# Performance work log

Measured on AMD Instinct MI355X. Metric: run time of the kernel, lower is better.

## Reference

```python
import jax, jax.numpy as jnp
import numpy as np

B = 64
D_MODEL = 2048
D_SSM = 4096      # expand * d_model
HEADDIM = 64
NHEADS = 64       # D_SSM // HEADDIM
D_STATE = 128
D_IN_PROJ = 2 * D_SSM + 2 * D_STATE + NHEADS  # 8512, d_mlp == 0
ACT_LEVELS = 2 ** (8 - 1) - 1  # 127
W_LEVELS = 2 ** (8 - 1) - 1


def fake_quant(x, levels):
    # symmetric absmax fake-quant along last dim with straight-through estimator
    scale = jnp.max(jnp.abs(x), axis=-1, keepdims=True) / levels
    scale = jnp.where(scale == 0, 1.0, scale)
    q = jnp.round(x / scale) * scale
    return x + jax.lax.stop_gradient(q - x)


def quant_linear(x, W):
    # QuantLinear: fake-quant activations (per row) and weights (per output channel)
    xq = fake_quant(x, ACT_LEVELS)
    Wq = fake_quant(W, W_LEVELS)
    return xq @ Wq.T


def softplus_taylor3(x):
    return jnp.log(2.0) + 0.5 * x + x ** 2 / 8.0 + x ** 3 / 48.0


def exp_taylor5(x):
    return 1.0 + x + x ** 2 / 2.0 + x ** 3 / 6.0 + x ** 4 / 24.0 + x ** 5 / 120.0


def setup_inputs() -> dict:
    key = jax.random.key(0)
    k = jax.random.split(key, 7)
    hidden_states = jax.random.normal(k[0], (B, 1, D_MODEL), dtype=jnp.float32)
    ssm_state = jax.random.normal(k[1], (B, NHEADS, HEADDIM, D_STATE), dtype=jnp.float32) * 0.1
    W_in = jax.random.normal(k[2], (D_IN_PROJ, D_MODEL), dtype=jnp.float32) * (1.0 / np.sqrt(D_MODEL))
    # dt_bias = inverse-softplus of dt ~ LogUniform(1e-3, 1e-1)
    dt = jnp.exp(jax.random.uniform(k[3], (NHEADS,)) * (np.log(0.1) - np.log(0.001)) + np.log(0.001))
    dt_bias = dt + jnp.log(-jnp.expm1(-dt))
    A_log = jnp.log(jax.random.uniform(k[4], (NHEADS,), minval=1.0, maxval=16.0))
    Dp = jnp.ones((D_SSM,), dtype=jnp.float32)
    W_out = jax.random.normal(k[5], (D_MODEL, D_SSM), dtype=jnp.float32) * (1.0 / np.sqrt(D_SSM))
    return {"hidden_states": hidden_states, "ssm_state": ssm_state, "W_in": W_in,
            "dt_bias": dt_bias, "A_log": A_log, "D": Dp, "W_out": W_out}


def reference(hidden_states, ssm_state, W_in, dt_bias, A_log, D, W_out):
    dtype = hidden_states.dtype
    b = hidden_states.shape[0]
    zxbcdt = quant_linear(hidden_states[:, 0, :], W_in)  # [b, 8512]
    z = zxbcdt[:, :D_SSM]
    xBC = zxbcdt[:, D_SSM:2 * D_SSM + 2 * D_STATE]
    dt = zxbcdt[:, -NHEADS:]
    # activation fake-quant on xBC (STE)
    xBC = fake_quant(xBC, ACT_LEVELS)
    x = xBC[:, :D_SSM]                                   # [b, d_ssm]
    Bm = xBC[:, D_SSM:D_SSM + D_STATE]                   # [b, n]
    C = xBC[:, D_SSM + D_STATE:]                         # [b, n]
    A = -jnp.exp(A_log.astype(jnp.float32))              # [h]
    # no_sftplus: piecewise 3rd-order Taylor softplus
    dt = dt + dt_bias.astype(dt.dtype)
    dt = jnp.where(dt < -2.0, 0.0, jnp.where(dt > 2.0, dt, softplus_taylor3(dt)))
    # taylor_exp: clipped 5th-order Taylor exp of dt*A
    dA = jnp.maximum(dt * A, -10000.0)
    scale = jnp.clip(exp_taylor5(dA), 0.0, 1.0)          # [b, h]
    xh = x.reshape(b, NHEADS, HEADDIM)                   # [b, h, p]
    dBx = jnp.einsum('bh,bn,bhp->bhpn', dt, Bm, xh)
    ssm_state = ssm_state * scale[:, :, None, None] + dBx  # [b, h, p, n]
    y = jnp.einsum('bhpn,bn->bhp', ssm_state.astype(dtype), C).reshape(b, D_SSM)
    y = fake_quant(y, ACT_LEVELS)
    y = y + D.astype(dtype) * x                          # per-channel skip (D has d_ssm entries)
    y = y * jax.nn.relu(z)
    y = fake_quant(y, ACT_LEVELS)
    out = quant_linear(y, W_out)                         # [b, d_model]
    return out[:, None, :]
```

## Files before the change

### kernel.cpp

```cpp
#include <hip/hip_runtime.h>


#define B_       64
#define DMODEL   2048
#define DSSM     4096
#define NH       64
#define HD       64
#define DSTATE   128
#define DPROJ    8512
#define XBCLEN   4352
#define KS1      8
#define KS2      16

typedef __attribute__((ext_vector_type(8))) short short8;
typedef __attribute__((ext_vector_type(4))) float floatx4;

__device__ __forceinline__ float blockMax256(float v, float* sm) {
  #pragma unroll
  for (int off = 32; off > 0; off >>= 1)
    v = fmaxf(v, __shfl_xor(v, off, 64));
  __syncthreads();
  if ((threadIdx.x & 63) == 0) sm[threadIdx.x >> 6] = v;
  __syncthreads();
  return fmaxf(fmaxf(sm[0], sm[1]), fmaxf(sm[2], sm[3]));
}

__device__ __forceinline__ float absmax4(float4 v) {
  return fmaxf(fmaxf(fabsf(v.x), fabsf(v.y)), fmaxf(fabsf(v.z), fabsf(v.w)));
}

__device__ __forceinline__ unsigned short bf16_of_int(float q) {
  return (unsigned short)(__float_as_uint(q) >> 16);
}

template<int COLS>
__device__ __forceinline__ void qrow(const float* __restrict__ in,
                                     unsigned short* __restrict__ outq,
                                     float* __restrict__ scales, int r, float* sm) {
  constexpr int NV = COLS / 1024;
  const float4* row = (const float4*)(in + (size_t)r * COLS);
  float4 v[NV];
  float m = 0.f;
  #pragma unroll
  for (int i = 0; i < NV; i++) {
    v[i] = row[threadIdx.x + i * 256];
    m = fmaxf(m, absmax4(v[i]));
  }
  float mx = blockMax256(m, sm);
  float s = mx * (1.0f / 127.0f);
  float rs = (s == 0.f) ? 0.f : 127.0f / mx;
  if (s == 0.f) s = 1.f;
  if (threadIdx.x == 0) scales[r] = s;
  unsigned short* orow = outq + (size_t)r * COLS;
  #pragma unroll
  for (int i = 0; i < NV; i++) {
    int idx = (threadIdx.x + i * 256) * 4;
    ushort4 o;
    o.x = bf16_of_int(rintf(v[i].x * rs));
    o.y = bf16_of_int(rintf(v[i].y * rs));
    o.z = bf16_of_int(rintf(v[i].z * rs));
    o.w = bf16_of_int(rintf(v[i].w * rs));
    *(ushort4*)(orow + idx) = o;
  }
}

__global__ __launch_bounds__(256) void kquant_all(
    const float* __restrict__ hidden, const float* __restrict__ W_in,
    const float* __restrict__ W_out,
    unsigned short* __restrict__ xq, unsigned short* __restrict__ winq,
    unsigned short* __restrict__ woq,
    float* __restrict__ sx, float* __restrict__ swin, float* __restrict__ swo) {
  __shared__ float sm[4];
  int bid = blockIdx.x;
  if (bid < DPROJ)                 qrow<DMODEL>(W_in, winq, swin, bid, sm);
  else if (bid < DPROJ + DMODEL)   qrow<DSSM>(W_out, woq, swo, bid - DPROJ, sm);
  else                             qrow<DMODEL>(hidden, xq, sx, bid - DPROJ - DMODEL, sm);
}

__global__ __launch_bounds__(256) void gemm_q(
    const unsigned short* __restrict__ A, int lda, const float* __restrict__ sA,
    const unsigned short* __restrict__ Bq, int ldb, const float* __restrict__ sB,
    float* __restrict__ Pout, int N, int kchunk) {
  int wave = threadIdx.x >> 6;
  int lane = threadIdx.x & 63;
  int l16 = lane & 15, quad = lane >> 4;
  int n0 = blockIdx.x * 64 + wave * 16;
  int k0 = blockIdx.y * kchunk;
  floatx4 zero = {0.f, 0.f, 0.f, 0.f};
  floatx4 acc[4] = {zero, zero, zero, zero};
  const unsigned short* brow = Bq + (size_t)(n0 + l16) * ldb + quad * 8;
  const unsigned short* arow = A + (size_t)l16 * lda + quad * 8;
  short8 bnext = *(const short8*)(brow + k0);
  short8 anext[4];
  #pragma unroll
  for (int mt = 0; mt < 4; mt++)
    anext[mt] = *(const short8*)(arow + (size_t)mt * 16 * lda + k0);
  for (int k = k0; k < k0 + kchunk; k += 32) {
    short8 bcur = bnext;
    short8 acur[4] = {anext[0], anext[1], anext[2], anext[3]};
    if (k + 32 < k0 + kchunk) {
      bnext = *(const short8*)(brow + k + 32);
      #pragma unroll
      for (int mt = 0; mt < 4; mt++)
        anext[mt] = *(const short8*)(arow + (size_t)mt * 16 * lda + k + 32);
    }
    #pragma unroll
    for (int mt = 0; mt < 4; mt++)
      acc[mt] = __builtin_amdgcn_mfma_f32_16x16x32_bf16(acur[mt], bcur, acc[mt], 0, 0, 0);
  }
  int ncol = n0 + l16;
  float sb = sB[ncol];
  float* pbase = Pout + (size_t)blockIdx.y * 64 * N;
  #pragma unroll
  for (int mt = 0; mt < 4; mt++) {
    #pragma unroll
    for (int r = 0; r < 4; r++) {
      int m = mt * 16 + quad * 4 + r;
      pbase[(size_t)m * N + ncol] = acc[mt][r] * sA[m] * sb;
    }
  }
}

__global__ __launch_bounds__(256) void kmid(
    const float* __restrict__ P1, const float* __restrict__ dt_bias,
    const float* __restrict__ A_log,
    float* __restrict__ zbuf, float* __restrict__ xbcq, float* __restrict__ coefs) {
  __shared__ float sm[4];
  __shared__ float dts[NH];
  __shared__ float sbc;
  int b = blockIdx.x, t = threadIdx.x;
  float4 v[9];
  float m = 0.f;
  #pragma unroll
  for (int i = 0; i < 9; i++) {
    int idx = t + i * 256;
    if (idx < 2128) {
      const float4* p0 = (const float4*)P1 + (size_t)b * 2128 + idx;
      float4 a = p0[0];
      #pragma unroll
      for (int s = 1; s < KS1; s++) {
        float4 q = p0[(size_t)s * 64 * 2128];
        a.x += q.x; a.y += q.y; a.z += q.z; a.w += q.w;
      }
      v[i] = a;
      if (idx >= 1024 && idx < 2112) m = fmaxf(m, absmax4(a));
      if (idx >= 2112) {
        dts[(t - 64) * 4 + 0] = a.x;
        dts[(t - 64) * 4 + 1] = a.y;
        dts[(t - 64) * 4 + 2] = a.z;
        dts[(t - 64) * 4 + 3] = a.w;
      }
    }
  }
  float mx = blockMax256(m, sm);
  float s = mx * (1.0f / 127.0f);
  float rs = (s == 0.f) ? 0.f : 127.0f / mx;
  if (s == 0.f) s = 1.f;
  float4 q8 = {0.f, 0.f, 0.f, 0.f};
  #pragma unroll
  for (int i = 0; i < 9; i++) {
    int idx = t + i * 256;
    if (idx < 1024) {
      *((float4*)(zbuf + (size_t)b * DSSM) + idx) = v[i];
    } else if (idx < 2112) {
      float4 q;
      q.x = rintf(v[i].x * rs) * s;
      q.y = rintf(v[i].y * rs) * s;
      q.z = rintf(v[i].z * rs) * s;
      q.w = rintf(v[i].w * rs) * s;
      if (i == 8) q8 = q;
      *((float4*)(xbcq + (size_t)b * XBCLEN) + (idx - 1024)) = q;
    }
  }
  float4 oth;
  oth.x = __shfl(q8.x, (t & 63) ^ 32, 64);
  oth.y = __shfl(q8.y, (t & 63) ^ 32, 64);
  oth.z = __shfl(q8.z, (t & 63) ^ 32, 64);
  oth.w = __shfl(q8.w, (t & 63) ^ 32, 64);
  float p = 0.f;
  if (t < 32) p = q8.x * oth.x + q8.y * oth.y + q8.z * oth.z + q8.w * oth.w;
  #pragma unroll
  for (int off = 1; off < 32; off <<= 1) p += __shfl_xor(p, off, 64);
  if (t == 0) sbc = p;
  __syncthreads();
  if (t < NH) {
    float dtv = dts[t] + dt_bias[t];
    if (dtv < -2.f) dtv = 0.f;
    else if (dtv <= 2.f)
      dtv = 0.6931471805599453f + 0.5f * dtv + dtv * dtv * (1.f / 8.f)
            + dtv * dtv * dtv * (1.f / 48.f);
    float A = -expf(A_log[t]);
    float dA = fmaxf(dtv * A, -10000.f);
    float e = 1.f + dA + dA * dA * (1.f / 2.f) + dA * dA * dA * (1.f / 6.f)
              + dA * dA * dA * dA * (1.f / 24.f)
              + dA * dA * dA * dA * dA * (1.f / 120.f);
    e = fminf(fmaxf(e, 0.f), 1.f);
    coefs[((size_t)b * NH + t) * 2 + 0] = e;
    coefs[((size_t)b * NH + t) * 2 + 1] = dtv * sbc;
  }
}

__global__ __launch_bounds__(256) void ky(const float* __restrict__ state,
                                          const float* __restrict__ xbcq,
                                          const float* __restrict__ coefs,
                                          float* __restrict__ yraw) {
  int h = blockIdx.x, b = blockIdx.y, t = threadIdx.x;
  const float* xrow = xbcq + (size_t)b * XBCLEN;
  const float* Cv = xrow + DSSM + DSTATE;
  int nc = (t & 15) * 8;
  float4 c4a = *(const float4*)(Cv + nc);
  float4 c4b = *(const float4*)(Cv + nc + 4);
  float2 cf = *(const float2*)(coefs + ((size_t)b * NH + h) * 2);
  const float4* st = (const float4*)(state + ((size_t)b * NH + h) * (HD * DSTATE));
  #pragma unroll
  for (int j = 0; j < 4; j++) {
    int r = j * 16 + (t >> 4);
    int base = r * 32 + (t & 15) * 2;
    float4 s0 = st[base], s1 = st[base + 1];
    float acc = s0.x * c4a.x + s0.y * c4a.y + s0.z * c4a.z + s0.w * c4a.w
              + s1.x * c4b.x + s1.y * c4b.y + s1.z * c4b.z + s1.w * c4b.w;
    #pragma unroll
    for (int off = 1; off < 16; off <<= 1) acc += __shfl_xor(acc, off, 64);
    if ((t & 15) == 0) {
      int d = h * HD + r;
      yraw[(size_t)b * DSSM + d] = cf.x * acc + cf.y * xrow[d];
    }
  }
}

__global__ __launch_bounds__(256) void kepi(const float* __restrict__ yraw,
                                            const float* __restrict__ zbuf,
                                            const float* __restrict__ xbcq,
                                            const float* __restrict__ Dv,
                                            unsigned short* __restrict__ q3,
                                            float* __restrict__ sy) {
  __shared__ float sm[4];
  int b = blockIdx.x, t = threadIdx.x;
  const float* yrow = yraw + (size_t)b * DSSM;
  float4 yv[4];
  float m = 0.f;
  #pragma unroll
  for (int i = 0; i < 4; i++) {
    yv[i] = *(const float4*)(yrow + t * 4 + i * 1024);
    m = fmaxf(m, absmax4(yv[i]));
  }
  float mx1 = blockMax256(m, sm);
  float s1 = mx1 * (1.0f / 127.0f);
  float rs1 = (s1 == 0.f) ? 0.f : 127.0f / mx1;
  if (s1 == 0.f) s1 = 1.f;
  float4 y3[4];
  float m2 = 0.f;
  #pragma unroll
  for (int i = 0; i < 4; i++) {
    int idx = t * 4 + i * 1024;
    float4 x4 = *(const float4*)(xbcq + (size_t)b * XBCLEN + idx);
    float4 z4 = *(const float4*)(zbuf + (size_t)b * DSSM + idx);
    float4 d4 = *(const float4*)(Dv + idx);
    float4 r;
    r.x = (rintf(yv[i].x * rs1) * s1 + d4.x * x4.x) * fmaxf(z4.x, 0.f);
    r.y = (rintf(yv[i].y * rs1) * s1 + d4.y * x4.y) * fmaxf(z4.y, 0.f);
    r.z = (rintf(yv[i].z * rs1) * s1 + d4.z * x4.z) * fmaxf(z4.z, 0.f);
    r.w = (rintf(yv[i].w * rs1) * s1 + d4.w * x4.w) * fmaxf(z4.w, 0.f);
    y3[i] = r;
    m2 = fmaxf(m2, absmax4(r));
  }
  float mx3 = blockMax256(m2, sm);
  float s3 = mx3 * (1.0f / 127.0f);
  float rs3 = (s3 == 0.f) ? 0.f : 127.0f / mx3;
  if (s3 == 0.f) s3 = 1.f;
  if (t == 0) sy[b] = s3;
  unsigned short* orow = q3 + (size_t)b * DSSM;
  #pragma unroll
  for (int i = 0; i < 4; i++) {
    int idx = t * 4 + i * 1024;
    ushort4 o;
    o.x = bf16_of_int(rintf(y3[i].x * rs3));
    o.y = bf16_of_int(rintf(y3[i].y * rs3));
    o.z = bf16_of_int(rintf(y3[i].z * rs3));
    o.w = bf16_of_int(rintf(y3[i].w * rs3));
    *(ushort4*)(orow + idx) = o;
  }
}

__global__ __launch_bounds__(256) void kout(const float* __restrict__ P2,
                                            float* __restrict__ out) {
  int idx = blockIdx.x * 256 + threadIdx.x;
  const float4* p = (const float4*)P2;
  float4 s = p[idx];
  #pragma unroll
  for (int i = 1; i < KS2; i++) {
    float4 a = p[(size_t)i * 32768 + idx];
    s.x += a.x; s.y += a.y; s.z += a.z; s.w += a.w;
  }
  ((float4*)out)[idx] = s;
}

extern "C" void kernel_launch(void* const* d_in, const int* in_sizes, int n_in,
                              void* d_out, int out_size, void* d_ws, size_t ws_size,
                              hipStream_t stream) {
  const float* hidden  = (const float*)d_in[0];
  const float* ssm     = (const float*)d_in[1];
  const float* W_in    = (const float*)d_in[2];
  const float* dt_bias = (const float*)d_in[3];
  const float* A_log   = (const float*)d_in[4];
  const float* Dv      = (const float*)d_in[5];
  const float* W_out   = (const float*)d_in[6];
  float* out = (float*)d_out;

  char* p = (char*)d_ws;
  auto alloc = [&](size_t bytes) {
    char* r = p;
    p += (bytes + 255) & ~(size_t)255;
    return r;
  };
  unsigned short* xq   = (unsigned short*)alloc((size_t)B_ * DMODEL * 2);
  unsigned short* winq = (unsigned short*)alloc((size_t)DPROJ * DMODEL * 2);
  unsigned short* woq  = (unsigned short*)alloc((size_t)DMODEL * DSSM * 2);
  unsigned short* q3   = (unsigned short*)alloc((size_t)B_ * DSSM * 2);
  float* sx    = (float*)alloc(B_ * 4);
  float* swin  = (float*)alloc(DPROJ * 4);
  float* swo   = (float*)alloc(DMODEL * 4);
  float* sy    = (float*)alloc(B_ * 4);
  float* P1    = (float*)alloc((size_t)KS1 * B_ * DPROJ * 4);
  float* P2    = (float*)alloc((size_t)KS2 * B_ * DMODEL * 4);
  float* zbuf  = (float*)alloc((size_t)B_ * DSSM * 4);
  float* xbcq  = (float*)alloc((size_t)B_ * XBCLEN * 4);
  float* coefs = (float*)alloc((size_t)B_ * NH * 2 * 4);
  float* yraw  = (float*)alloc((size_t)B_ * DSSM * 4);

  kquant_all<<<DPROJ + DMODEL + B_, 256, 0, stream>>>(hidden, W_in, W_out,
                                                      xq, winq, woq, sx, swin, swo);
  gemm_q<<<dim3(DPROJ / 64, KS1), 256, 0, stream>>>(xq, DMODEL, sx,
                                                    winq, DMODEL, swin,
                                                    P1, DPROJ, DMODEL / KS1);
  kmid<<<B_, 256, 0, stream>>>(P1, dt_bias, A_log, zbuf, xbcq, coefs);
  ky<<<dim3(NH, B_), 256, 0, stream>>>(ssm, xbcq, coefs, yraw);
  kepi<<<B_, 256, 0, stream>>>(yraw, zbuf, xbcq, Dv, q3, sy);
  gemm_q<<<dim3(DMODEL / 64, KS2), 256, 0, stream>>>(q3, DSSM, sy,
                                                     woq, DSSM, swo,
                                                     P2, DMODEL, DSSM / KS2);
  kout<<<DMODEL / 16, 256, 0, stream>>>(P2, out);
}
```

Before: 324.3 us.

## Switch quantized GEMMs from bf16 to int8 MFMA and coalesce ky state reads

Quantized activations and weights are stored as packed int8 instead of bf16-encoded integers, and both GEMMs use the i32 16x16x64 int8 MFMA, which halves the bytes written and read for weights and activations. The rounded values fit in [-127,127], so int32 accumulation should be exact. The ky kernel is also reshaped so each thread reads one contiguous float4 of state per iteration, with 32-lane reductions. The main cost still left is the fp32 read of the weights during quantization.

```diff
diff --git a/kernel.cpp b/kernel.cpp
--- a/kernel.cpp
+++ b/kernel.cpp
@@ -12,8 +12,7 @@
 #define KS1      8
 #define KS2      16
 
-typedef __attribute__((ext_vector_type(8))) short short8;
-typedef __attribute__((ext_vector_type(4))) float floatx4;
+typedef __attribute__((ext_vector_type(4))) int int4v;
 
 __device__ __forceinline__ float blockMax256(float v, float* sm) {
   #pragma unroll
@@ -29,14 +28,18 @@
   return fmaxf(fmaxf(fabsf(v.x), fabsf(v.y)), fmaxf(fabsf(v.z), fabsf(v.w)));
 }
 
-__device__ __forceinline__ unsigned short bf16_of_int(float q) {
-  return (unsigned short)(__float_as_uint(q) >> 16);
+__device__ __forceinline__ unsigned int pack4(float a, float b, float c, float d,
+                                              float rs) {
+  int c0 = (int)rintf(a * rs), c1 = (int)rintf(b * rs);
+  int c2 = (int)rintf(c * rs), c3 = (int)rintf(d * rs);
+  return (unsigned)(c0 & 255) | ((unsigned)(c1 & 255) << 8) |
+         ((unsigned)(c2 & 255) << 16) | ((unsigned)(c3 & 255) << 24);
 }
 
 template<int COLS>
-__device__ __forceinline__ void qrow(const float* __restrict__ in,
-                                     unsigned short* __restrict__ outq,
-                                     float* __restrict__ scales, int r, float* sm) {
+__device__ __forceinline__ void qrow8(const float* __restrict__ in,
+                                      unsigned int* __restrict__ outq,
+                                      float* __restrict__ scales, int r, float* sm) {
   constexpr int NV = COLS / 1024;
   const float4* row = (const float4*)(in + (size_t)r * COLS);
   float4 v[NV];
@@ -51,62 +54,55 @@
   float rs = (s == 0.f) ? 0.f : 127.0f / mx;
   if (s == 0.f) s = 1.f;
   if (threadIdx.x == 0) scales[r] = s;
-  unsigned short* orow = outq + (size_t)r * COLS;
-  #pragma unroll
-  for (int i = 0; i < NV; i++) {
-    int idx = (threadIdx.x + i * 256) * 4;
-    ushort4 o;
-    o.x = bf16_of_int(rintf(v[i].x * rs));
-    o.y = bf16_of_int(rintf(v[i].y * rs));
-    o.z = bf16_of_int(rintf(v[i].z * rs));
-    o.w = bf16_of_int(rintf(v[i].w * rs));
-    *(ushort4*)(orow + idx) = o;
-  }
+  unsigned int* orow = outq + (size_t)r * (COLS / 4);
+  #pragma unroll
+  for (int i = 0; i < NV; i++)
+    orow[threadIdx.x + i * 256] = pack4(v[i].x, v[i].y, v[i].z, v[i].w, rs);
 }
 
 __global__ __launch_bounds__(256) void kquant_all(
     const float* __restrict__ hidden, const float* __restrict__ W_in,
     const float* __restrict__ W_out,
-    unsigned short* __restrict__ xq, unsigned short* __restrict__ winq,
-    unsigned short* __restrict__ woq,
+    unsigned int* __restrict__ xq, unsigned int* __restrict__ winq,
+    unsigned int* __restrict__ woq,
     float* __restrict__ sx, float* __restrict__ swin, float* __restrict__ swo) {
   __shared__ float sm[4];
   int bid = blockIdx.x;
-  if (bid < DPROJ)                 qrow<DMODEL>(W_in, winq, swin, bid, sm);
-  else if (bid < DPROJ + DMODEL)   qrow<DSSM>(W_out, woq, swo, bid - DPROJ, sm);
-  else                             qrow<DMODEL>(hidden, xq, sx, bid - DPROJ - DMODEL, sm);
-}
-
-__global__ __launch_bounds__(256) void gemm_q(
-    const unsigned short* __restrict__ A, int lda, const float* __restrict__ sA,
-    const unsigned short* __restrict__ Bq, int ldb, const float* __restrict__ sB,
+  if (bid < DPROJ)                 qrow8<DMODEL>(W_in, winq, swin, bid, sm);
+  else if (bid < DPROJ + DMODEL)   qrow8<DSSM>(W_out, woq, swo, bid - DPROJ, sm);
+  else                             qrow8<DMODEL>(hidden, xq, sx, bid - DPROJ - DMODEL, sm);
+}
+
+__global__ __launch_bounds__(256) void gemm_q8(
+    const char* __restrict__ A, int lda, const float* __restrict__ sA,
+    const char* __restrict__ Bq, int ldb, const float* __restrict__ sB,
     float* __restrict__ Pout, int N, int kchunk) {
   int wave = threadIdx.x >> 6;
   int lane = threadIdx.x & 63;
   int l16 = lane & 15, quad = lane >> 4;
   int n0 = blockIdx.x * 64 + wave * 16;
   int k0 = blockIdx.y * kchunk;
-  floatx4 zero = {0.f, 0.f, 0.f, 0.f};
-  floatx4 acc[4] = {zero, zero, zero, zero};
-  const unsigned short* brow = Bq + (size_t)(n0 + l16) * ldb + quad * 8;
-  const unsigned short* arow = A + (size_t)l16 * lda + quad * 8;
-  short8 bnext = *(const short8*)(brow + k0);
-  short8 anext[4];
+  int4v zero = {0, 0, 0, 0};
+  int4v acc[4] = {zero, zero, zero, zero};
+  const char* brow = Bq + (size_t)(n0 + l16) * ldb + quad * 16;
+  const char* arow = A + (size_t)l16 * lda + quad * 16;
+  int4v bnext = *(const int4v*)(brow + k0);
+  int4v anext[4];
   #pragma unroll
   for (int mt = 0; mt < 4; mt++)
-    anext[mt] = *(const short8*)(arow + (size_t)mt * 16 * lda + k0);
-  for (int k = k0; k < k0 + kchunk; k += 32) {
-    short8 bcur = bnext;
-    short8 acur[4] = {anext[0], anext[1], anext[2], anext[3]};
-    if (k + 32 < k0 + kchunk) {
-      bnext = *(const short8*)(brow + k + 32);
+    anext[mt] = *(const int4v*)(arow + (size_t)mt * 16 * lda + k0);
+  for (int k = k0; k < k0 + kchunk; k += 64) {
+    int4v bcur = bnext;
+    int4v acur[4] = {anext[0], anext[1], anext[2], anext[3]};
+    if (k + 64 < k0 + kchunk) {
+      bnext = *(const int4v*)(brow + k + 64);
       #pragma unroll
       for (int mt = 0; mt < 4; mt++)
-        anext[mt] = *(const short8*)(arow + (size_t)mt * 16 * lda + k + 32);
+        anext[mt] = *(const int4v*)(arow + (size_t)mt * 16 * lda + k + 64);
     }
     #pragma unroll
     for (int mt = 0; mt < 4; mt++)
-      acc[mt] = __builtin_amdgcn_mfma_f32_16x16x32_bf16(acur[mt], bcur, acc[mt], 0, 0, 0);
+      acc[mt] = __builtin_amdgcn_mfma_i32_16x16x64_i8(acur[mt], bcur, acc[mt], 0, 0, 0);
   }
   int ncol = n0 + l16;
   float sb = sB[ncol];
@@ -116,7 +112,7 @@
     #pragma unroll
     for (int r = 0; r < 4; r++) {
       int m = mt * 16 + quad * 4 + r;
-      pbase[(size_t)m * N + ncol] = acc[mt][r] * sA[m] * sb;
+      pbase[(size_t)m * N + ncol] = (float)acc[mt][r] * sA[m] * sb;
     }
   }
 }
@@ -207,21 +203,17 @@
   int h = blockIdx.x, b = blockIdx.y, t = threadIdx.x;
   const float* xrow = xbcq + (size_t)b * XBCLEN;
   const float* Cv = xrow + DSSM + DSTATE;
-  int nc = (t & 15) * 8;
-  float4 c4a = *(const float4*)(Cv + nc);
-  float4 c4b = *(const float4*)(Cv + nc + 4);
+  float4 c4 = *(const float4*)(Cv + (t & 31) * 4);
   float2 cf = *(const float2*)(coefs + ((size_t)b * NH + h) * 2);
   const float4* st = (const float4*)(state + ((size_t)b * NH + h) * (HD * DSTATE));
   #pragma unroll
-  for (int j = 0; j < 4; j++) {
-    int r = j * 16 + (t >> 4);
-    int base = r * 32 + (t & 15) * 2;
-    float4 s0 = st[base], s1 = st[base + 1];
-    float acc = s0.x * c4a.x + s0.y * c4a.y + s0.z * c4a.z + s0.w * c4a.w
-              + s1.x * c4b.x + s1.y * c4b.y + s1.z * c4b.z + s1.w * c4b.w;
+  for (int j = 0; j < 8; j++) {
+    float4 s4 = st[j * 256 + t];
+    float acc = s4.x * c4.x + s4.y * c4.y + s4.z * c4.z + s4.w * c4.w;
     #pragma unroll
-    for (int off = 1; off < 16; off <<= 1) acc += __shfl_xor(acc, off, 64);
-    if ((t & 15) == 0) {
+    for (int off = 1; off < 32; off <<= 1) acc += __shfl_xor(acc, off, 64);
+    if ((t & 31) == 0) {
+      int r = j * 8 + (t >> 5);
       int d = h * HD + r;
       yraw[(size_t)b * DSSM + d] = cf.x * acc + cf.y * xrow[d];
     }
@@ -232,7 +224,7 @@
                                             const float* __restrict__ zbuf,
                                             const float* __restrict__ xbcq,
                                             const float* __restrict__ Dv,
-                                            unsigned short* __restrict__ q3,
+                                            unsigned int* __restrict__ q3,
                                             float* __restrict__ sy) {
   __shared__ float sm[4];
   int b = blockIdx.x, t = threadIdx.x;
@@ -269,17 +261,10 @@
   float rs3 = (s3 == 0.f) ? 0.f : 127.0f / mx3;
   if (s3 == 0.f) s3 = 1.f;
   if (t == 0) sy[b] = s3;
-  unsigned short* orow = q3 + (size_t)b * DSSM;
-  #pragma unroll
-  for (int i = 0; i < 4; i++) {
-    int idx = t * 4 + i * 1024;
-    ushort4 o;
-    o.x = bf16_of_int(rintf(y3[i].x * rs3));
-    o.y = bf16_of_int(rintf(y3[i].y * rs3));
-    o.z = bf16_of_int(rintf(y3[i].z * rs3));
-    o.w = bf16_of_int(rintf(y3[i].w * rs3));
-    *(ushort4*)(orow + idx) = o;
-  }
+  unsigned int* orow = q3 + (size_t)b * (DSSM / 4);
+  #pragma unroll
+  for (int i = 0; i < 4; i++)
+    orow[t + i * 256] = pack4(y3[i].x, y3[i].y, y3[i].z, y3[i].w, rs3);
 }
 
 __global__ __launch_bounds__(256) void kout(const float* __restrict__ P2,
@@ -313,10 +298,10 @@
     p += (bytes + 255) & ~(size_t)255;
     return r;
   };
-  unsigned short* xq   = (unsigned short*)alloc((size_t)B_ * DMODEL * 2);
-  unsigned short* winq = (unsigned short*)alloc((size_t)DPROJ * DMODEL * 2);
-  unsigned short* woq  = (unsigned short*)alloc((size_t)DMODEL * DSSM * 2);
-  unsigned short* q3   = (unsigned short*)alloc((size_t)B_ * DSSM * 2);
+  unsigned int* xq   = (unsigned int*)alloc((size_t)B_ * DMODEL);
+  unsigned int* winq = (unsigned int*)alloc((size_t)DPROJ * DMODEL);
+  unsigned int* woq  = (unsigned int*)alloc((size_t)DMODEL * DSSM);
+  unsigned int* q3   = (unsigned int*)alloc((size_t)B_ * DSSM);
   float* sx    = (float*)alloc(B_ * 4);
   float* swin  = (float*)alloc(DPROJ * 4);
   float* swo   = (float*)alloc(DMODEL * 4);
@@ -330,14 +315,14 @@
 
   kquant_all<<<DPROJ + DMODEL + B_, 256, 0, stream>>>(hidden, W_in, W_out,
                                                       xq, winq, woq, sx, swin, swo);
-  gemm_q<<<dim3(DPROJ / 64, KS1), 256, 0, stream>>>(xq, DMODEL, sx,
-                                                    winq, DMODEL, swin,
-                                                    P1, DPROJ, DMODEL / KS1);
+  gemm_q8<<<dim3(DPROJ / 64, KS1), 256, 0, stream>>>((const char*)xq, DMODEL, sx,
+                                                     (const char*)winq, DMODEL, swin,
+                                                     P1, DPROJ, DMODEL / KS1);
   kmid<<<B_, 256, 0, stream>>>(P1, dt_bias, A_log, zbuf, xbcq, coefs);
   ky<<<dim3(NH, B_), 256, 0, stream>>>(ssm, xbcq, coefs, yraw);
   kepi<<<B_, 256, 0, stream>>>(yraw, zbuf, xbcq, Dv, q3, sy);
-  gemm_q<<<dim3(DMODEL / 64, KS2), 256, 0, stream>>>(q3, DSSM, sy,
-                                                     woq, DSSM, swo,
-                                                     P2, DMODEL, DSSM / KS2);
+  gemm_q8<<<dim3(DMODEL / 64, KS2), 256, 0, stream>>>((const char*)q3, DSSM, sy,
+                                                      (const char*)woq, DSSM, swo,
+                                                      P2, DMODEL, DSSM / KS2);
   kout<<<DMODEL / 16, 256, 0, stream>>>(P2, out);
 }
```

After: 309.1 us. 4.7% less time.
